# Kernel tuning notes

Measured on AMD Instinct MI355X. Metric: run time of the kernel, lower is better.

## Reference

```python
import jax, jax.numpy as jnp
import numpy as np

EPS = 1e-6
DROP_RATE = 0.25

def setup_inputs() -> dict:
    key = jax.random.key(0)
    k1, k2, k3 = jax.random.split(key, 3)
    B, S, D = 4, 2048, 2048
    inputs = jax.random.normal(k1, (B, S, D), dtype=jnp.float32)
    # keras 'uniform' initializer: U(-0.05, 0.05)
    W_1 = jax.random.uniform(k2, (D, D), dtype=jnp.float32, minval=-0.05, maxval=0.05)
    W_2 = jax.random.uniform(k3, (D, D), dtype=jnp.float32, minval=-0.05, maxval=0.05)
    return {"inputs": inputs, "W_1": W_1, "W_2": W_2}

def reference(inputs, W_1, W_2):
    # LayerNorm over last axis (no affine: gamma/beta unused in original call)
    mean = jnp.mean(inputs, axis=-1, keepdims=True)
    var = jnp.mean(jnp.square(inputs - mean), axis=-1, keepdims=True)
    x_norm = (inputs - mean) / jnp.sqrt(var + EPS)          # [B,S,D]
    # 2-layer MLP with relu
    h = jax.nn.relu(jnp.einsum('bsd,de->bse', x_norm, W_1))  # [B,S,D]
    y = jnp.einsum('bsd,de->bse', h, W_2)                    # [B,S,D]
    # dropout(0.25), inverted scaling, fixed key for determinism
    keep = jax.random.bernoulli(jax.random.key(1), 1.0 - DROP_RATE, y.shape)
    y_drop = jnp.where(keep, y / (1.0 - DROP_RATE), 0.0)
    return x_norm + y_drop
```

## Files before the change

kernel.cpp:

```cpp
#include <hip/hip_runtime.h>
#include <hip/hip_bf16.h>
#include <stdint.h>

#define M_DIM 8192
#define N_DIM 2048
#define K_DIM 2048

typedef __bf16 bf16x8_t __attribute__((ext_vector_type(8)));
typedef float f32x4_t __attribute__((ext_vector_type(4)));

__device__ __forceinline__ unsigned tf_rotl(unsigned x, int r) {
  return (x << r) | (x >> (32 - r));
}
__device__ __forceinline__ unsigned threefry_mask_bits(unsigned ctr) {
  unsigned x0 = 0u, x1 = ctr;
  const unsigned ks0 = 0u, ks1 = 1u, ks2 = 0x1BD11BDBu;
  x0 += ks0; x1 += ks1;
#define TFR(r) { x0 += x1; x1 = tf_rotl(x1, (r)); x1 ^= x0; }
  TFR(13) TFR(15) TFR(26) TFR(6)
  x0 += ks1; x1 += ks2 + 1u;
  TFR(17) TFR(29) TFR(16) TFR(24)
  x0 += ks2; x1 += ks0 + 2u;
  TFR(13) TFR(15) TFR(26) TFR(6)
  x0 += ks0; x1 += ks1 + 3u;
  TFR(17) TFR(29) TFR(16) TFR(24)
  x0 += ks1; x1 += ks2 + 4u;
  TFR(13) TFR(15) TFR(26) TFR(6)
  x0 += ks2; x1 += ks0 + 5u;
#undef TFR
  return x0 ^ x1;
}

__device__ __forceinline__ void gload_lds16(const __hip_bfloat16* g, unsigned short* l) {
  __builtin_amdgcn_global_load_lds(
      (const __attribute__((address_space(1))) unsigned int*)g,
      (__attribute__((address_space(3))) unsigned int*)l,
      16, 0, 0);
}

__global__ __launch_bounds__(256) void wt_kernel(
    const float* __restrict__ W1, const float* __restrict__ W2,
    __hip_bfloat16* __restrict__ W1t, __hip_bfloat16* __restrict__ W2t) {
  __shared__ float tile[32][33];
  const float* src = blockIdx.z ? W2 : W1;
  __hip_bfloat16* dst = blockIdx.z ? W2t : W1t;
  int x = blockIdx.x * 32 + threadIdx.x;
  int y = blockIdx.y * 32 + threadIdx.y;
#pragma unroll
  for (int i = 0; i < 32; i += 8)
    tile[threadIdx.y + i][threadIdx.x] = src[(size_t)(y + i) * N_DIM + x];
  __syncthreads();
  int xo = blockIdx.y * 32 + threadIdx.x;
  int yo = blockIdx.x * 32 + threadIdx.y;
#pragma unroll
  for (int i = 0; i < 32; i += 8)
    dst[(size_t)(yo + i) * K_DIM + xo] = __float2bfloat16(tile[threadIdx.x][threadIdx.y + i]);
}

__global__ __launch_bounds__(256) void ln_kernel(const float* __restrict__ X,
                                                 __hip_bfloat16* __restrict__ Xn) {
  const int row = blockIdx.x;
  const float4* xv = (const float4*)(X + (size_t)row * K_DIM);
  float4 v0 = xv[threadIdx.x];
  float4 v1 = xv[threadIdx.x + 256];
  float s  = v0.x + v0.y + v0.z + v0.w + v1.x + v1.y + v1.z + v1.w;
  float ss = v0.x*v0.x + v0.y*v0.y + v0.z*v0.z + v0.w*v0.w
           + v1.x*v1.x + v1.y*v1.y + v1.z*v1.z + v1.w*v1.w;
#pragma unroll
  for (int off = 32; off > 0; off >>= 1) {
    s  += __shfl_xor(s, off);
    ss += __shfl_xor(ss, off);
  }
  __shared__ float rs[4], rss[4];
  const int wave = threadIdx.x >> 6;
  if ((threadIdx.x & 63) == 0) { rs[wave] = s; rss[wave] = ss; }
  __syncthreads();
  float S  = rs[0] + rs[1] + rs[2] + rs[3];
  float SS = rss[0] + rss[1] + rss[2] + rss[3];
  float mean = S * (1.0f / 2048.0f);
  float var  = SS * (1.0f / 2048.0f) - mean * mean;
  float rstd = 1.0f / sqrtf(var + 1e-6f);
  float vv[8] = {v0.x, v0.y, v0.z, v0.w, v1.x, v1.y, v1.z, v1.w};
  unsigned short o[8];
#pragma unroll
  for (int i = 0; i < 8; i++) {
    __hip_bfloat16 b = __float2bfloat16((vv[i] - mean) * rstd);
    o[i] = *(unsigned short*)&b;
  }
  ushort4* dst = (ushort4*)(Xn + (size_t)row * K_DIM);
  dst[threadIdx.x]       = make_ushort4(o[0], o[1], o[2], o[3]);
  dst[threadIdx.x + 256] = make_ushort4(o[4], o[5], o[6], o[7]);
}

template <int EPI>
__global__ __launch_bounds__(256) void gemm128(
    const __hip_bfloat16* __restrict__ A,
    const __hip_bfloat16* __restrict__ Bt,
    const __hip_bfloat16* __restrict__ Xn,
    __hip_bfloat16* __restrict__ Hout,
    float* __restrict__ Fout) {
  __shared__ unsigned short As[2][128 * 64];
  __shared__ unsigned short Bs[2][128 * 64];
  const int tid  = threadIdx.x;
  const int lane = tid & 63;
  const int wave = tid >> 6;
  const int wm = wave >> 1, wn = wave & 1;
  const int mBase = blockIdx.x * 128;
  const int nBase = blockIdx.y * 128;

  f32x4_t acc[4][4];
#pragma unroll
  for (int i = 0; i < 4; i++)
#pragma unroll
    for (int j = 0; j < 4; j++) acc[i][j] = (f32x4_t){0.f, 0.f, 0.f, 0.f};

  const int rowIn  = lane >> 3;
  const int csrc   = ((lane & 7) ^ (rowIn & 7)) << 3;
  const __hip_bfloat16* aSrc[4];
  const __hip_bfloat16* bSrc[4];
  int sDst[4];
#pragma unroll
  for (int j = 0; j < 4; j++) {
    const int ca = wave + 4 * j;
    aSrc[j] = A  + (size_t)(mBase + 8 * ca + rowIn) * K_DIM + csrc;
    bSrc[j] = Bt + (size_t)(nBase + 8 * ca + rowIn) * K_DIM + csrc;
    sDst[j] = ca * 512;
  }

  const int fr = lane & 15;
  const int fq = lane >> 4;
  const int sw = fr & 7;
  const int cA0 = (fq ^ sw) * 8;
  const int cA1 = ((4 | fq) ^ sw) * 8;
  const int rowOffA = (wm * 64 + fr) * 64;
  const int rowOffB = (wn * 64 + fr) * 64;

#define STAGE(buf, k0)                                        \
  {                                                           \
    _Pragma("unroll")                                         \
    for (int j = 0; j < 4; j++) {                             \
      gload_lds16(aSrc[j] + (k0), &As[buf][sDst[j]]);         \
      gload_lds16(bSrc[j] + (k0), &Bs[buf][sDst[j]]);         \
    }                                                         \
  }

#define COMPUTE_HALF(buf, cOff)                                                 \
  {                                                                             \
    bf16x8_t af[4], bfr[4];                                                     \
    _Pragma("unroll")                                                           \
    for (int i = 0; i < 4; i++) af[i]  = *(const bf16x8_t*)(&As[buf][rowOffA + i * 1024 + (cOff)]); \
    _Pragma("unroll")                                                           \
    for (int i = 0; i < 4; i++) bfr[i] = *(const bf16x8_t*)(&Bs[buf][rowOffB + i * 1024 + (cOff)]); \
    _Pragma("unroll")                                                           \
    for (int mi = 0; mi < 4; mi++)                                              \
      _Pragma("unroll")                                                         \
      for (int ni = 0; ni < 4; ni++)                                            \
        acc[mi][ni] = __builtin_amdgcn_mfma_f32_16x16x32_bf16(af[mi], bfr[ni], acc[mi][ni], 0, 0, 0); \
  }
#define COMPUTE(buf) { COMPUTE_HALF(buf, cA0) COMPUTE_HALF(buf, cA1) }

  STAGE(0, 0)
  for (int k0 = 0; k0 < K_DIM - 128; k0 += 128) {
    __syncthreads();
    STAGE(1, k0 + 64)
    COMPUTE(0)
    __syncthreads();
    STAGE(0, k0 + 128)
    COMPUTE(1)
  }
  __syncthreads();
  STAGE(1, K_DIM - 64)
  COMPUTE(0)
  __syncthreads();
  COMPUTE(1)
#undef STAGE
#undef COMPUTE
#undef COMPUTE_HALF

  const int mRow = mBase + wm * 64;
  const int nCol = nBase + wn * 64;
#pragma unroll
  for (int mi = 0; mi < 4; mi++) {
#pragma unroll
    for (int ni = 0; ni < 4; ni++) {
      const int n  = nCol + ni * 16 + fr;
      const int m0 = mRow + mi * 16 + fq * 4;
#pragma unroll
      for (int r = 0; r < 4; r++) {
        float v = acc[mi][ni][r];
        size_t j = (size_t)(m0 + r) * N_DIM + n;
        if (EPI == 0) {
          Hout[j] = __float2bfloat16(fmaxf(v, 0.0f));
        } else {
          unsigned bits = threefry_mask_bits((unsigned)j);
          float y  = (bits < 0xC0000000u) ? v * (1.0f / 0.75f) : 0.0f;
          Fout[j]  = __bfloat162float(Xn[j]) + y;
        }
      }
    }
  }
}

extern "C" void kernel_launch(void* const* d_in, const int* in_sizes, int n_in,
                              void* d_out, int out_size, void* d_ws, size_t ws_size,
                              hipStream_t stream) {
  (void)in_sizes; (void)n_in; (void)out_size; (void)ws_size;
  const float* X  = (const float*)d_in[0];
  const float* W1 = (const float*)d_in[1];
  const float* W2 = (const float*)d_in[2];
  float* out = (float*)d_out;

  unsigned char* ws = (unsigned char*)d_ws;
  __hip_bfloat16* Xn  = (__hip_bfloat16*)(ws);
  __hip_bfloat16* H   = (__hip_bfloat16*)(ws + ((size_t)32 << 20));
  __hip_bfloat16* W1t = (__hip_bfloat16*)(ws + ((size_t)64 << 20));
  __hip_bfloat16* W2t = (__hip_bfloat16*)(ws + ((size_t)72 << 20));

  wt_kernel<<<dim3(64, 64, 2), dim3(32, 8, 1), 0, stream>>>(W1, W2, W1t, W2t);
  ln_kernel<<<M_DIM, 256, 0, stream>>>(X, Xn);
  gemm128<0><<<dim3(M_DIM / 128, N_DIM / 128), 256, 0, stream>>>(Xn, W1t, nullptr, H, nullptr);
  gemm128<1><<<dim3(M_DIM / 128, N_DIM / 128), 256, 0, stream>>>(H, W2t, Xn, nullptr, out);
}
```

Measured before the change: 319.5 us.

## Rewrite GEMMs as 256x256 tiles with 8 waves and fine-grained pipelined schedule

Replaces the 128x128, 4-wave GEMM with a 256x256, 8-wave block tile. It uses a 1D grid with a remapped block order for L2 locality and a hand-scheduled loop that interleaves LDS reads, async global-to-LDS loads and MFMA quarters. Explicit waitcnt, barriers and setprio are used to overlap memory with compute. This aims to raise arithmetic intensity and hide load latency, but relies on fragile manual wait counts and uses more registers and LDS per block, which can lower occupancy.

After: 342.5 us. +7.2%, slower.

```diff
diff --git a/kernel.cpp b/kernel.cpp
--- a/kernel.cpp
+++ b/kernel.cpp
@@ -93,101 +93,150 @@
 }
 
 template <int EPI>
-__global__ __launch_bounds__(256) void gemm128(
+__global__ __launch_bounds__(512, 2) void gemm256(
     const __hip_bfloat16* __restrict__ A,
     const __hip_bfloat16* __restrict__ Bt,
     const __hip_bfloat16* __restrict__ Xn,
     __hip_bfloat16* __restrict__ Hout,
     float* __restrict__ Fout) {
-  __shared__ unsigned short As[2][128 * 64];
-  __shared__ unsigned short Bs[2][128 * 64];
+  __shared__ unsigned short As[2][16384];
+  __shared__ unsigned short Bs[2][16384];
   const int tid  = threadIdx.x;
   const int lane = tid & 63;
   const int wave = tid >> 6;
-  const int wm = wave >> 1, wn = wave & 1;
-  const int mBase = blockIdx.x * 128;
-  const int nBase = blockIdx.y * 128;
-
-  f32x4_t acc[4][4];
-#pragma unroll
-  for (int i = 0; i < 4; i++)
+  const int wm = wave >> 2;
+  const int wn = wave & 3;
+
+  const int bid = blockIdx.x;
+  const int wg  = (bid & 7) * 32 + (bid >> 3);
+  const int mBase = (wg & 31) << 8;
+  const int nBase = (wg >> 5) << 8;
+
+  f32x4_t acc[8][4];
+#pragma unroll
+  for (int i = 0; i < 8; i++)
 #pragma unroll
     for (int j = 0; j < 4; j++) acc[i][j] = (f32x4_t){0.f, 0.f, 0.f, 0.f};
 
-  const int rowIn  = lane >> 3;
-  const int csrc   = ((lane & 7) ^ (rowIn & 7)) << 3;
-  const __hip_bfloat16* aSrc[4];
-  const __hip_bfloat16* bSrc[4];
-  int sDst[4];
-#pragma unroll
-  for (int j = 0; j < 4; j++) {
-    const int ca = wave + 4 * j;
-    aSrc[j] = A  + (size_t)(mBase + 8 * ca + rowIn) * K_DIM + csrc;
-    bSrc[j] = Bt + (size_t)(nBase + 8 * ca + rowIn) * K_DIM + csrc;
-    sDst[j] = ca * 512;
-  }
+  const int rowIn = lane >> 3;
+  const int csrc  = ((lane & 7) ^ (rowIn & 7)) << 3;
+  const __hip_bfloat16* aSrcB = A  + (size_t)(mBase + 8 * wave + rowIn) * K_DIM + csrc;
+  const int bRowW = ((wave >> 2) << 6) + ((wave & 3) << 3);
+  const __hip_bfloat16* bSrcB = Bt + (size_t)(nBase + bRowW + rowIn) * K_DIM + csrc;
+  const int aDst = wave << 9;
+  const int bDst = bRowW << 6;
+
+#define STA(b, h, k)                                                                         \
+  gload_lds16(aSrcB + (size_t)((h) * 64) * K_DIM + (k), &As[b][aDst + (h) * 4096]);          \
+  gload_lds16(aSrcB + (size_t)((h) * 64 + 128) * K_DIM + (k), &As[b][aDst + (h) * 4096 + 8192]);
+#define STB(b, h, k)                                                                         \
+  gload_lds16(bSrcB + (size_t)((h) * 32) * K_DIM + (k), &Bs[b][bDst + (h) * 2048]);          \
+  gload_lds16(bSrcB + (size_t)((h) * 32 + 128) * K_DIM + (k), &Bs[b][bDst + (h) * 2048 + 8192]);
 
   const int fr = lane & 15;
   const int fq = lane >> 4;
-  const int sw = fr & 7;
-  const int cA0 = (fq ^ sw) * 8;
-  const int cA1 = ((4 | fq) ^ sw) * 8;
-  const int rowOffA = (wm * 64 + fr) * 64;
-  const int rowOffB = (wn * 64 + fr) * 64;
-
-#define STAGE(buf, k0)                                        \
-  {                                                           \
-    _Pragma("unroll")                                         \
-    for (int j = 0; j < 4; j++) {                             \
-      gload_lds16(aSrc[j] + (k0), &As[buf][sDst[j]]);         \
-      gload_lds16(bSrc[j] + (k0), &Bs[buf][sDst[j]]);         \
-    }                                                         \
-  }
-
-#define COMPUTE_HALF(buf, cOff)                                                 \
-  {                                                                             \
-    bf16x8_t af[4], bfr[4];                                                     \
-    _Pragma("unroll")                                                           \
-    for (int i = 0; i < 4; i++) af[i]  = *(const bf16x8_t*)(&As[buf][rowOffA + i * 1024 + (cOff)]); \
-    _Pragma("unroll")                                                           \
-    for (int i = 0; i < 4; i++) bfr[i] = *(const bf16x8_t*)(&Bs[buf][rowOffB + i * 1024 + (cOff)]); \
-    _Pragma("unroll")                                                           \
-    for (int mi = 0; mi < 4; mi++)                                              \
-      _Pragma("unroll")                                                         \
-      for (int ni = 0; ni < 4; ni++)                                            \
-        acc[mi][ni] = __builtin_amdgcn_mfma_f32_16x16x32_bf16(af[mi], bfr[ni], acc[mi][ni], 0, 0, 0); \
-  }
-#define COMPUTE(buf) { COMPUTE_HALF(buf, cA0) COMPUTE_HALF(buf, cA1) }
-
-  STAGE(0, 0)
-  for (int k0 = 0; k0 < K_DIM - 128; k0 += 128) {
-    __syncthreads();
-    STAGE(1, k0 + 64)
-    COMPUTE(0)
-    __syncthreads();
-    STAGE(0, k0 + 128)
-    COMPUTE(1)
-  }
-  __syncthreads();
-  STAGE(1, K_DIM - 64)
-  COMPUTE(0)
-  __syncthreads();
-  COMPUTE(1)
-#undef STAGE
-#undef COMPUTE
-#undef COMPUTE_HALF
-
-  const int mRow = mBase + wm * 64;
-  const int nCol = nBase + wn * 64;
-#pragma unroll
-  for (int mi = 0; mi < 4; mi++) {
-#pragma unroll
-    for (int ni = 0; ni < 4; ni++) {
-      const int n  = nCol + ni * 16 + fr;
-      const int m0 = mRow + mi * 16 + fq * 4;
+  const int c0 = ((fq)     ^ (fr & 7)) << 3;
+  const int c1 = ((4 | fq) ^ (fr & 7)) << 3;
+  const int aRd = (wm * 128 + fr) * 64;
+  const int bRd = (wn * 64  + fr) * 64;
+
+  bf16x8_t aF[4][2], bF[4][2];
+#define RDA(b, f)                                                      \
+  aF[(f) & 3][0] = *(const bf16x8_t*)&As[b][aRd + (f) * 1024 + c0];    \
+  aF[(f) & 3][1] = *(const bf16x8_t*)&As[b][aRd + (f) * 1024 + c1];
+#define RDB(b, nf)                                                     \
+  bF[nf][0] = *(const bf16x8_t*)&Bs[b][bRd + (nf) * 1024 + c0];        \
+  bF[nf][1] = *(const bf16x8_t*)&Bs[b][bRd + (nf) * 1024 + c1];
+
+#define MFMAQ(mh, nlo)                                                             \
+  _Pragma("unroll")                                                                \
+  for (int mi = 0; mi < 4; mi++) {                                                 \
+    _Pragma("unroll")                                                              \
+    for (int nj = 0; nj < 2; nj++) {                                               \
+      acc[(mh) * 4 + mi][(nlo) + nj] = __builtin_amdgcn_mfma_f32_16x16x32_bf16(    \
+          aF[mi][0], bF[(nlo) + nj][0], acc[(mh) * 4 + mi][(nlo) + nj], 0, 0, 0);  \
+      acc[(mh) * 4 + mi][(nlo) + nj] = __builtin_amdgcn_mfma_f32_16x16x32_bf16(    \
+          aF[mi][1], bF[(nlo) + nj][1], acc[(mh) * 4 + mi][(nlo) + nj], 0, 0, 0);  \
+    }                                                                              \
+  }
+
+#define BAR() __builtin_amdgcn_s_barrier()
+#define LGKM0()                                              \
+  {                                                          \
+    asm volatile("s_waitcnt lgkmcnt(0)" ::: "memory");       \
+    __builtin_amdgcn_sched_barrier(0);                       \
+  }
+#define LGKM8() asm volatile("s_waitcnt lgkmcnt(8)" ::: "memory")
+#define VMW(n)                                               \
+  {                                                          \
+    asm volatile("s_waitcnt vmcnt(" #n ")" ::: "memory");    \
+    __builtin_amdgcn_sched_barrier(0);                       \
+  }
+
+#define TILE(t, S1, S2, S3, S4, VMODE)                                   \
+  {                                                                      \
+    const int buf = (t) & 1;                                             \
+     \
+    RDA(buf, 0) RDA(buf, 1) RDA(buf, 2) RDA(buf, 3)                      \
+    RDB(buf, 0) RDB(buf, 1)                                              \
+    if (S1) { STB(buf ^ 1, 1, ((t) + 1) * 64) }                          \
+    LGKM8(); BAR(); LGKM0();                                             \
+    __builtin_amdgcn_s_setprio(1); MFMAQ(0, 0)                           \
+    __builtin_amdgcn_s_setprio(0); BAR();                                \
+     \
+    RDB(buf, 2) RDB(buf, 3)                                              \
+    if (S2) { STA(buf, 0, ((t) + 2) * 64) }                              \
+    BAR(); LGKM0();                                                      \
+    __builtin_amdgcn_s_setprio(1); MFMAQ(0, 2)                           \
+    __builtin_amdgcn_s_setprio(0); BAR();                                \
+     \
+    RDA(buf, 4) RDA(buf, 5) RDA(buf, 6) RDA(buf, 7)                      \
+    if (S3) { STB(buf, 0, ((t) + 2) * 64) }                              \
+    BAR(); LGKM0();                                                      \
+    __builtin_amdgcn_s_setprio(1); MFMAQ(1, 0)                           \
+    __builtin_amdgcn_s_setprio(0); BAR();                                \
+    \
+    if (S4) { STA(buf, 1, ((t) + 2) * 64) }                              \
+    if ((VMODE) == 0) { VMW(6); } else if ((VMODE) == 1) { VMW(0); }     \
+    BAR();                                                               \
+    __builtin_amdgcn_s_setprio(1); MFMAQ(1, 2)                           \
+    __builtin_amdgcn_s_setprio(0); BAR();                                \
+  }
+
+  STA(0, 0, 0) STB(0, 0, 0) STA(0, 1, 0) STB(0, 1, 0)
+  VMW(4);
+  STA(1, 0, 64) STB(1, 0, 64) STA(1, 1, 64)
+  VMW(6);
+  BAR();
+
+  for (int t = 0; t < 30; ++t) {
+    TILE(t, 1, 1, 1, 1, 0)
+  }
+  TILE(30, 1, 0, 0, 0, 1)
+  TILE(31, 0, 0, 0, 0, 2)
+
+#undef TILE
+#undef STA
+#undef STB
+#undef RDA
+#undef RDB
+#undef MFMAQ
+#undef BAR
+#undef LGKM0
+#undef LGKM8
+#undef VMW
+
+  const int mW = mBase + wm * 128 + fq * 4;
+  const int nW = nBase + wn * 64 + fr;
+#pragma unroll
+  for (int f = 0; f < 8; f++) {
+#pragma unroll
+    for (int nf = 0; nf < 4; nf++) {
+      const int n  = nW + nf * 16;
+      const int m0 = mW + f * 16;
 #pragma unroll
       for (int r = 0; r < 4; r++) {
-        float v = acc[mi][ni][r];
+        float v = acc[f][nf][r];
         size_t j = (size_t)(m0 + r) * N_DIM + n;
         if (EPI == 0) {
           Hout[j] = __float2bfloat16(fmaxf(v, 0.0f));
@@ -218,6 +267,6 @@
 
   wt_kernel<<<dim3(64, 64, 2), dim3(32, 8, 1), 0, stream>>>(W1, W2, W1t, W2t);
   ln_kernel<<<M_DIM, 256, 0, stream>>>(X, Xn);
-  gemm128<0><<<dim3(M_DIM / 128, N_DIM / 128), 256, 0, stream>>>(Xn, W1t, nullptr, H, nullptr);
-  gemm128<1><<<dim3(M_DIM / 128, N_DIM / 128), 256, 0, stream>>>(H, W2t, Xn, nullptr, out);
-}
+  gemm256<0><<<dim3(256, 1, 1), dim3(512, 1, 1), 0, stream>>>(Xn, W1t, nullptr, H, nullptr);
+  gemm256<1><<<dim3(256, 1, 1), dim3(512, 1, 1), 0, stream>>>(H, W2t, Xn, nullptr, out);
+}
```

## Deepen GEMM LDS prefetch with explicit vmcnt waits and raw barriers

Applied to the files above, without the earlier changes.

Restructures the GEMM main loop so two K-tiles are in flight: both buffers are staged up front, and after computing each buffer its refill for two steps ahead is issued. Waits use partial s_waitcnt vmcnt(8) so the previous stage's loads can stay outstanding while the current one is consumed. Bare s_barrier replaces __syncthreads to avoid the compiler's full waits. The risk is correctness, since it depends on the vmcnt count matching the 8 direct-to-LDS loads per stage, and on the barriers ordering the LDS reads before the overwrite.

Result: no change. 315.6 us (-1.2%).

```diff
diff --git a/kernel.cpp b/kernel.cpp
--- a/kernel.cpp
+++ b/kernel.cpp
@@ -159,23 +159,36 @@
   }
 #define COMPUTE(buf) { COMPUTE_HALF(buf, cA0) COMPUTE_HALF(buf, cA1) }
 
+#define BAR() __builtin_amdgcn_s_barrier()
+#define VMW(n)  asm volatile("s_waitcnt vmcnt(" #n ")" ::: "memory")
+
+#define TSTEP(BUF, STG, KNEXT, VMODE)                                    \
+  {                                                                      \
+    COMPUTE(BUF)                                                         \
+    BAR();                               \
+    if (STG) { STAGE(BUF, KNEXT) }                                       \
+    if ((VMODE) == 0) { VMW(8); } else if ((VMODE) == 1) { VMW(0); }     \
+    if ((VMODE) != 2) { BAR(); }              \
+  }
+
   STAGE(0, 0)
-  for (int k0 = 0; k0 < K_DIM - 128; k0 += 128) {
-    __syncthreads();
-    STAGE(1, k0 + 64)
-    COMPUTE(0)
-    __syncthreads();
-    STAGE(0, k0 + 128)
-    COMPUTE(1)
-  }
-  __syncthreads();
-  STAGE(1, K_DIM - 64)
-  COMPUTE(0)
-  __syncthreads();
-  COMPUTE(1)
+  STAGE(1, 64)
+  VMW(8);
+  BAR();
+
+  for (int k0 = 0; k0 < 1920; k0 += 128) {
+    TSTEP(0, 1, k0 + 128, 0)
+    TSTEP(1, 1, k0 + 192, 0)
+  }
+  TSTEP(0, 0, 0, 1)
+  TSTEP(1, 0, 0, 2)
+
+#undef TSTEP
 #undef STAGE
 #undef COMPUTE
 #undef COMPUTE_HALF
+#undef BAR
+#undef VMW
 
   const int mRow = mBase + wm * 64;
   const int nCol = nBase + wn * 64;
```
